# Kernel optimization log

Hardware: AMD Instinct MI355X
Metric: run time of the kernel (lower is better)

Reference implementation:

```python
import jax, jax.numpy as jnp
import numpy as np

B, S, H = 2, 2048, 2048
NH, HD = 16, 128


def _rope_tables(seq_len, dim, base=10000.0):
    inv_freq = 1.0 / (base ** (np.arange(0, dim, 2, dtype=np.float32) / dim))
    t = np.arange(seq_len, dtype=np.float32)
    freqs = np.outer(t, inv_freq)                      # [S, dim/2]
    emb = np.concatenate([freqs, freqs], axis=-1)      # [S, dim] (HF convention)
    return jnp.asarray(np.cos(emb)), jnp.asarray(np.sin(emb))


def setup_inputs() -> dict:
    key = jax.random.key(0)
    k1, k2, k3, k4, k5 = jax.random.split(key, 5)
    hidden_states = jax.random.normal(k1, (B, S, H), dtype=jnp.float32)
    # additive causal mask, broadcast over heads: (B, 1, S, S)
    causal = jnp.tril(jnp.ones((S, S), dtype=bool))
    attention_mask = jnp.where(causal, 0.0, -1e9).astype(jnp.float32)
    attention_mask = jnp.broadcast_to(attention_mask[None, None], (B, 1, S, S))
    rope_cos, rope_sin = _rope_tables(S, HD)
    scale = 1.0 / np.sqrt(H)
    Wq = jax.random.normal(k2, (H, H), dtype=jnp.float32) * scale
    Wk = jax.random.normal(k3, (H, H), dtype=jnp.float32) * scale
    Wv = jax.random.normal(k4, (H, H), dtype=jnp.float32) * scale
    Wo = jax.random.normal(k5, (H, H), dtype=jnp.float32) * scale
    return dict(hidden_states=hidden_states, attention_mask=attention_mask,
                rope_cos=rope_cos, rope_sin=rope_sin, Wq=Wq, Wk=Wk, Wv=Wv, Wo=Wo)


def _rotate_half(x):
    half = x.shape[-1] // 2
    return jnp.concatenate([-x[..., half:], x[..., :half]], axis=-1)


def reference(hidden_states, attention_mask, rope_cos, rope_sin, Wq, Wk, Wv, Wo):
    bsz, q_len, _ = hidden_states.shape
    scaling = HD ** -0.5
    # projections (torch Linear: y = x @ W.T)
    q = (hidden_states @ Wq.T).reshape(bsz, q_len, NH, HD).transpose(0, 2, 1, 3)
    k = (hidden_states @ Wk.T).reshape(bsz, q_len, NH, HD).transpose(0, 2, 1, 3)
    v = (hidden_states @ Wv.T).reshape(bsz, q_len, NH, HD).transpose(0, 2, 1, 3)
    # RoPE (rotate_half convention)
    cos = rope_cos[None, None]  # [1,1,S,HD]
    sin = rope_sin[None, None]
    q = q * cos + _rotate_half(q) * sin
    k = k * cos + _rotate_half(k) * sin
    # attention
    scores = jnp.einsum('bhqd,bhkd->bhqk', q, k) * scaling + attention_mask
    attn = jax.nn.softmax(scores.astype(jnp.float32), axis=-1).astype(q.dtype)
    out = jnp.einsum('bhqk,bhkd->bhqd', attn, v)
    out = out.transpose(0, 2, 1, 3).reshape(bsz, q_len, NH * HD)
    return out @ Wo.T
```

## Files before the change

kernel.cpp:

```cpp
#include <hip/hip_runtime.h>
#include <hip/hip_bf16.h>

typedef __bf16 bf16;
typedef __attribute__((ext_vector_type(8))) __bf16 bf16x8;
typedef __attribute__((ext_vector_type(4))) __bf16 bf16x4;
typedef __attribute__((ext_vector_type(4))) float f32x4;

#define BB 2
#define SS 2048
#define HH 2048
#define NH 16
#define HD 128

#define GLOAD_LDS16(g, l)                                                  \
    __builtin_amdgcn_global_load_lds(                                      \
        (const __attribute__((address_space(1))) void*)(g),                \
        (__attribute__((address_space(3))) void*)(l), 16, 0, 0)

__global__ __launch_bounds__(256) void cast_all(const float* __restrict__ hs,
                                                const float* __restrict__ Wq,
                                                const float* __restrict__ Wk,
                                                const float* __restrict__ Wv,
                                                const float* __restrict__ Wo,
                                                bf16* __restrict__ Xb,
                                                bf16* __restrict__ Wqkv,
                                                bf16* __restrict__ Wob) {
    const int XE4 = (BB * SS * HH) / 4;
    const int WE4 = (HH * HH) / 4;
    int i = blockIdx.x * 256 + threadIdx.x;
    const float* src;
    bf16* dst;
    int off;
    if (i < XE4) { src = hs; dst = Xb; off = i; }
    else if (i < XE4 + WE4) { src = Wq; dst = Wqkv; off = i - XE4; }
    else if (i < XE4 + 2 * WE4) { src = Wk; dst = Wqkv + (size_t)HH * HH; off = i - XE4 - WE4; }
    else if (i < XE4 + 3 * WE4) { src = Wv; dst = Wqkv + 2 * (size_t)HH * HH; off = i - XE4 - 2 * WE4; }
    else { src = Wo; dst = Wob; off = i - XE4 - 3 * WE4; }
    f32x4 v = *reinterpret_cast<const f32x4*>(src + (size_t)off * 4);
    bf16x4 o;
    o[0] = (bf16)v[0]; o[1] = (bf16)v[1]; o[2] = (bf16)v[2]; o[3] = (bf16)v[3];
    *reinterpret_cast<bf16x4*>(dst + (size_t)off * 4) = o;
}

__global__ __launch_bounds__(512, 2) void gemm256_qkv(const bf16* __restrict__ A,
                                                      const bf16* __restrict__ B,
                                                      bf16* __restrict__ Cb,
                                                      int M, int N, int K) {
    __shared__ bf16 LA[2][256 * 64];
    __shared__ bf16 LB[2][192 * 64];
    const int tid = threadIdx.x, lane = tid & 63, wave = tid >> 6;
    const int l15 = lane & 15, lhi = lane >> 4;
    const int wr = wave >> 2, wc = wave & 3;
    const int NBY = M >> 8;
    const int cpx = gridDim.x >> 3;
    const int wg = (blockIdx.x & 7) * cpx + (blockIdx.x >> 3);
    const int m0 = (wg & 15) * 256, n0 = (wg >> 4) * 192;
    const int NK = K >> 6;
    const int xorR = (l15 & 7) << 4;

    auto stageA = [&](int buf, int t, int h) {
        const int k0 = t << 6;
#pragma unroll
        for (int j = 0; j < 2; ++j) {
            int Xw = (h * 128 + j * 64 + wave * 8) << 7;
            int X = Xw + lane * 16;
            int T = X ^ (((X >> 7) & 7) << 4);
            GLOAD_LDS16(&A[(size_t)(m0 + (T >> 7)) * K + k0 + ((T & 127) >> 1)],
                        (char*)LA[buf] + Xw);
        }
    };
    auto stageB = [&](int buf, int t, int s) {
        const int k0 = t << 6;
        int row_base = (wave >> 1) * 48 + s * 16 + (wave & 1) * 8;
        int Xw = row_base << 7;
        int X = Xw + lane * 16;
        int T = X ^ (((X >> 7) & 7) << 4);
        GLOAD_LDS16(&B[(size_t)(n0 + (T >> 7)) * K + k0 + ((T & 127) >> 1)],
                    (char*)LB[buf] + Xw);
    };

    f32x4 acc[8][3] = {};

    stageA(0, 0, 0); stageA(0, 0, 1);
    stageB(0, 0, 0); stageB(0, 0, 1); stageB(0, 0, 2);
    stageA(1, 1, 0); stageA(1, 1, 1);
    stageB(1, 1, 0); stageB(1, 1, 1);
    asm volatile("s_waitcnt vmcnt(6)" ::: "memory");
    __builtin_amdgcn_s_barrier();

    bf16x8 af[8][2], bv[2];

#pragma unroll 1
    for (int t = 0; t < NK; ++t) {
        const int buf = t & 1;
        char* lA = (char*)LA[buf];
        char* lB = (char*)LB[buf];

#pragma unroll
        for (int mf = 0; mf < 8; ++mf)
#pragma unroll
            for (int ks = 0; ks < 2; ++ks) {
                int T = ((wr * 128 + mf * 16 + l15) << 7) + ks * 64 + lhi * 16;
                af[mf][ks] = *reinterpret_cast<const bf16x8*>(lA + (T ^ xorR));
            }
#pragma unroll
        for (int ks = 0; ks < 2; ++ks) {
            int T = ((wc * 48 + l15) << 7) + ks * 64 + lhi * 16;
            bv[ks] = *reinterpret_cast<const bf16x8*>(lB + (T ^ xorR));
        }
        if (t + 1 < NK) stageB(buf ^ 1, t + 1, 2);
        __builtin_amdgcn_s_barrier();
        __builtin_amdgcn_s_setprio(1);
#pragma unroll
        for (int mf = 0; mf < 8; ++mf)
#pragma unroll
            for (int ks = 0; ks < 2; ++ks)
                acc[mf][0] = __builtin_amdgcn_mfma_f32_16x16x32_bf16(af[mf][ks], bv[ks], acc[mf][0], 0, 0, 0);
        __builtin_amdgcn_s_setprio(0);
        __builtin_amdgcn_s_barrier();

#pragma unroll
        for (int ks = 0; ks < 2; ++ks) {
            int T = ((wc * 48 + 16 + l15) << 7) + ks * 64 + lhi * 16;
            bv[ks] = *reinterpret_cast<const bf16x8*>(lB + (T ^ xorR));
        }
        if (t + 2 < NK) { stageB(buf, t + 2, 0); stageA(buf, t + 2, 0); }
        __builtin_amdgcn_s_barrier();
        __builtin_amdgcn_s_setprio(1);
#pragma unroll
        for (int mf = 0; mf < 8; ++mf)
#pragma unroll
            for (int ks = 0; ks < 2; ++ks)
                acc[mf][1] = __builtin_amdgcn_mfma_f32_16x16x32_bf16(af[mf][ks], bv[ks], acc[mf][1], 0, 0, 0);
        __builtin_amdgcn_s_setprio(0);
        __builtin_amdgcn_s_barrier();

#pragma unroll
        for (int ks = 0; ks < 2; ++ks) {
            int T = ((wc * 48 + 32 + l15) << 7) + ks * 64 + lhi * 16;
            bv[ks] = *reinterpret_cast<const bf16x8*>(lB + (T ^ xorR));
        }
        if (t + 2 < NK) { stageB(buf, t + 2, 1); stageA(buf, t + 2, 1); }
        __builtin_amdgcn_s_barrier();
        __builtin_amdgcn_s_setprio(1);
#pragma unroll
        for (int mf = 0; mf < 8; ++mf)
#pragma unroll
            for (int ks = 0; ks < 2; ++ks)
                acc[mf][2] = __builtin_amdgcn_mfma_f32_16x16x32_bf16(af[mf][ks], bv[ks], acc[mf][2], 0, 0, 0);
        __builtin_amdgcn_s_setprio(0);
        if (t + 2 < NK) {
            asm volatile("s_waitcnt vmcnt(6)" ::: "memory");
        } else if (t + 2 == NK) {
            asm volatile("s_waitcnt vmcnt(0)" ::: "memory");
        }
        __builtin_amdgcn_s_barrier();
    }

#pragma unroll
    for (int mf = 0; mf < 8; ++mf)
#pragma unroll
        for (int nsl = 0; nsl < 3; ++nsl)
#pragma unroll
            for (int r = 0; r < 4; ++r) {
                int gm = m0 + wr * 128 + mf * 16 + lhi * 4 + r;
                int gn = n0 + wc * 48 + nsl * 16 + l15;
                int proj = gn >> 11, n2 = gn & 2047;
                int b = gm >> 11, s = gm & (SS - 1);
                int h = n2 >> 7, d = n2 & (HD - 1);
                Cb[((size_t)proj << 23) + ((((size_t)(b * NH + h)) * SS + s) << 7) + d] =
                    (bf16)acc[mf][nsl][r];
            }
}

__global__ __launch_bounds__(256) void gemm_bt(const bf16* __restrict__ A,
                                               const bf16* __restrict__ B,
                                               float* __restrict__ Cf,
                                               int M, int N, int K) {
    __shared__ bf16 As[128 * 64];
    __shared__ bf16 Bs[128 * 64];
    const int tid = threadIdx.x;
    const int lane = tid & 63, wave = tid >> 6;
    const int l15 = lane & 15, lhi = lane >> 4;
    const int m0 = blockIdx.y * 128, n0 = blockIdx.x * 128;
    const int wm = (wave >> 1) * 64, wn = (wave & 1) * 64;
    const int lrow = lane >> 3;
    const int lcol = (lane & 7) * 8;

    f32x4 acc[4][4] = {};

    for (int k0 = 0; k0 < K; k0 += 64) {
#pragma unroll
        for (int j = 0; j < 4; ++j) {
            const int c = wave * 4 + j;
            const int row = c * 8 + lrow;
            GLOAD_LDS16(&A[(size_t)(m0 + row) * K + k0 + lcol], &As[c * 512]);
            GLOAD_LDS16(&B[(size_t)(n0 + row) * K + k0 + lcol], &Bs[c * 512]);
        }
        __syncthreads();
#pragma unroll
        for (int ks = 0; ks < 2; ++ks) {
            bf16x8 af[4], bfr[4];
#pragma unroll
            for (int i = 0; i < 4; ++i)
                af[i] = *reinterpret_cast<const bf16x8*>(&As[(wm + i * 16 + l15) * 64 + ks * 32 + 8 * lhi]);
#pragma unroll
            for (int j = 0; j < 4; ++j)
                bfr[j] = *reinterpret_cast<const bf16x8*>(&Bs[(wn + j * 16 + l15) * 64 + ks * 32 + 8 * lhi]);
#pragma unroll
            for (int i = 0; i < 4; ++i)
#pragma unroll
                for (int j = 0; j < 4; ++j)
                    acc[i][j] = __builtin_amdgcn_mfma_f32_16x16x32_bf16(af[i], bfr[j], acc[i][j], 0, 0, 0);
        }
        __syncthreads();
    }

#pragma unroll
    for (int i = 0; i < 4; ++i)
#pragma unroll
        for (int j = 0; j < 4; ++j)
#pragma unroll
            for (int r = 0; r < 4; ++r) {
                int gm = m0 + wm + i * 16 + lhi * 4 + r;
                int gn = n0 + wn + j * 16 + l15;
                Cf[(size_t)gm * N + gn] = acc[i][j][r];
            }
}

__global__ __launch_bounds__(256) void rope_tv(bf16* __restrict__ Qh,
                                               bf16* __restrict__ Kh,
                                               const float* __restrict__ cosT,
                                               const float* __restrict__ sinT,
                                               const bf16* __restrict__ Vh,
                                               bf16* __restrict__ Vt) {
    __shared__ bf16 T[64 * 64];
    const int tid = threadIdx.x;
    if (blockIdx.x < 2048) {
        int idx = blockIdx.x * 256 + tid;
        int g = idx & 7;
        int s = (idx >> 3) & (SS - 1);
        int head = idx >> 14;
        int d0 = g * 8;
        size_t base = ((size_t)head * SS + s) * HD;
        f32x4 ca = *reinterpret_cast<const f32x4*>(&cosT[s * HD + d0]);
        f32x4 cb = *reinterpret_cast<const f32x4*>(&cosT[s * HD + d0 + 4]);
        f32x4 sa = *reinterpret_cast<const f32x4*>(&sinT[s * HD + d0]);
        f32x4 sb = *reinterpret_cast<const f32x4*>(&sinT[s * HD + d0 + 4]);
        bf16x8 ql = *reinterpret_cast<const bf16x8*>(&Qh[base + d0]);
        bf16x8 qh = *reinterpret_cast<const bf16x8*>(&Qh[base + 64 + d0]);
        bf16x8 kl = *reinterpret_cast<const bf16x8*>(&Kh[base + d0]);
        bf16x8 kh = *reinterpret_cast<const bf16x8*>(&Kh[base + 64 + d0]);
        bf16x8 qlo, qhi, klo, khi;
#pragma unroll
        for (int j = 0; j < 8; ++j) {
            float c = (j < 4) ? ca[j] : cb[j - 4];
            float sn = (j < 4) ? sa[j] : sb[j - 4];
            float q0 = (float)ql[j], q1 = (float)qh[j];
            float k0 = (float)kl[j], k1 = (float)kh[j];
            qlo[j] = (bf16)(q0 * c - q1 * sn);
            qhi[j] = (bf16)(q1 * c + q0 * sn);
            klo[j] = (bf16)(k0 * c - k1 * sn);
            khi[j] = (bf16)(k1 * c + k0 * sn);
        }
        *reinterpret_cast<bf16x8*>(&Qh[base + d0]) = qlo;
        *reinterpret_cast<bf16x8*>(&Qh[base + 64 + d0]) = qhi;
        *reinterpret_cast<bf16x8*>(&Kh[base + d0]) = klo;
        *reinterpret_cast<bf16x8*>(&Kh[base + 64 + d0]) = khi;
    } else {
        const int b2 = blockIdx.x - 2048;
        const int s0 = (b2 & 31) * 64;
        const int d0 = ((b2 >> 5) & 1) * 64;
        const int head = b2 >> 6;
        const bf16* src = Vh + ((size_t)head * SS) * HD;
        bf16* dst = Vt + ((size_t)head * HD) * SS;

#pragma unroll
        for (int i = 0; i < 2; ++i) {
            int id = tid + i * 256;
            int r = id >> 3, c16 = id & 7;
            bf16x8 v = *reinterpret_cast<const bf16x8*>(&src[(size_t)(s0 + r) * HD + d0 + c16 * 8]);
            int sw = c16 ^ ((r ^ (r >> 3)) & 7);
            *reinterpret_cast<bf16x8*>((char*)T + r * 128 + sw * 16) = v;
        }
        __syncthreads();
#pragma unroll
        for (int i = 0; i < 2; ++i) {
            int id = tid + i * 256;
            int dr = id >> 3, sc8 = (id & 7) * 8;
            bf16x8 o;
#pragma unroll
            for (int j = 0; j < 8; ++j) {
                int r = sc8 + j;
                int sw = (dr >> 3) ^ ((r ^ (r >> 3)) & 7);
                o[j] = *reinterpret_cast<const bf16*>((char*)T + r * 128 + sw * 16 + (dr & 7) * 2);
            }
            *reinterpret_cast<bf16x8*>(&dst[(size_t)(d0 + dr) * SS + s0 + sc8]) = o;
        }
    }
}

__global__ __launch_bounds__(512) void attn_kernel(const bf16* __restrict__ Q,
                                                   const bf16* __restrict__ K,
                                                   const bf16* __restrict__ Vt,
                                                   bf16* __restrict__ Ob) {
    __shared__ bf16 Ks[2][64 * 128];
    __shared__ bf16 Vs[2][128 * 64];
    __shared__ bf16 Ps[8][16 * 72];

    const int tid = threadIdx.x, lane = tid & 63, wave = tid >> 6;
    const int l15 = lane & 15, lhi = lane >> 4;
    const int bid = blockIdx.x;
    const int orig = (bid & 7) * 32 + (bid >> 3);
    const int head = orig >> 3;
    const int pi = orig & 7;
    const int b = head >> 4, h = head & (NH - 1);
    const size_t hb = (size_t)head * SS * HD;
    const bf16* Vth = Vt + (size_t)head * HD * SS;
    const float cexp = 0.08838834764831845f * 1.4426950408889634f;
    const float THR = 62.0f;

    auto stageKV = [&](int buf, int kv0) {
#pragma unroll
        for (int j = 0; j < 2; ++j) {
            int Xw = (j * 8 + wave) << 10;
            int X = Xw + lane * 16;
            int T = X ^ (((X >> 8) & 7) << 4);
            GLOAD_LDS16(&K[hb + (size_t)(kv0 + (T >> 8)) * HD + ((T & 255) >> 1)],
                        (char*)Ks[buf] + Xw);
        }
#pragma unroll
        for (int j = 0; j < 2; ++j) {
            int Xw = (j * 8 + wave) << 10;
            int X = Xw + lane * 16;
            int T = X ^ (((X >> 7) & 7) << 4);
            GLOAD_LDS16(&Vth[(size_t)(T >> 7) * SS + kv0 + ((T & 127) >> 1)],
                        (char*)Vs[buf] + Xw);
        }
    };

#pragma unroll 1
    for (int part = 0; part < 2; ++part) {
        const int t = part ? (15 - pi) : pi;
        const int q0 = t * 128;
        const int qw = q0 + wave * 16;
        const int nkv = 2 * t + 2;

        bf16x8 qf[4];
#pragma unroll
        for (int ks = 0; ks < 4; ++ks)
            qf[ks] = *reinterpret_cast<const bf16x8*>(
                &Q[hb + (size_t)(qw + l15) * HD + ks * 32 + 8 * lhi]);

        f32x4 oacc[8] = {};
        float Mr[4], Lp[4];
#pragma unroll
        for (int r = 0; r < 4; ++r) { Mr[r] = -INFINITY; Lp[r] = 0.f; }

        stageKV(0, 0);
        asm volatile("s_waitcnt vmcnt(0)" ::: "memory");
        __builtin_amdgcn_s_barrier();

        for (int it = 0; it < nkv; ++it) {
            const int cur = it & 1;
            if (it + 1 < nkv) stageKV(cur ^ 1, (it + 1) * 64);

            f32x4 sf[4] = {};
#pragma unroll
            for (int ks = 0; ks < 4; ++ks) {
#pragma unroll
                for (int ne = 0; ne < 4; ++ne) {
                    int row = ne * 16 + l15;
                    bf16x8 kf = *reinterpret_cast<const bf16x8*>(
                        (const char*)Ks[cur] + ((row * 256 + (ks * 4 + lhi) * 16) ^ ((row & 7) << 4)));
                    sf[ne] = __builtin_amdgcn_mfma_f32_16x16x32_bf16(qf[ks], kf, sf[ne], 0, 0, 0);
                }
            }

            if (it >= nkv - 2) {
#pragma unroll
                for (int ne = 0; ne < 4; ++ne)
#pragma unroll
                    for (int r = 0; r < 4; ++r) {
                        int gq = qw + lhi * 4 + r;
                        int gk = it * 64 + ne * 16 + l15;
                        if (gk > gq) sf[ne][r] = -INFINITY;
                    }
            }

            float lm[4];
#pragma unroll
            for (int r = 0; r < 4; ++r)
                lm[r] = fmaxf(fmaxf(sf[0][r], sf[1][r]), fmaxf(sf[2][r], sf[3][r]));
            bool need = (lm[0] > Mr[0] + THR) || (lm[1] > Mr[1] + THR) ||
                        (lm[2] > Mr[2] + THR) || (lm[3] > Mr[3] + THR);
            if (__any(need)) {
                float rmax[4] = {lm[0], lm[1], lm[2], lm[3]};
#pragma unroll
                for (int m = 1; m < 16; m <<= 1)
#pragma unroll
                    for (int r = 0; r < 4; ++r)
                        rmax[r] = fmaxf(rmax[r], __shfl_xor(rmax[r], m));
#pragma unroll
                for (int r = 0; r < 4; ++r) {
                    float nM = fmaxf(Mr[r], rmax[r]);
                    float scf = __builtin_amdgcn_exp2f((Mr[r] - nM) * cexp);
                    Mr[r] = nM;
                    Lp[r] *= scf;
#pragma unroll
                    for (int nf = 0; nf < 8; ++nf) oacc[nf][r] *= scf;
                }
            }
#pragma unroll
            for (int ne = 0; ne < 4; ++ne)
#pragma unroll
                for (int r = 0; r < 4; ++r) {
                    float p = __builtin_amdgcn_exp2f((sf[ne][r] - Mr[r]) * cexp);
                    Lp[r] += p;
                    Ps[wave][(lhi * 4 + r) * 72 + ne * 16 + l15] = (bf16)p;
                }

#pragma unroll
            for (int ks = 0; ks < 2; ++ks) {
                bf16x8 pa = *reinterpret_cast<const bf16x8*>(
                    &Ps[wave][l15 * 72 + ks * 32 + 8 * lhi]);
#pragma unroll
                for (int nf = 0; nf < 8; ++nf) {
                    int row = nf * 16 + l15;
                    bf16x8 vb = *reinterpret_cast<const bf16x8*>(
                        (const char*)Vs[cur] + ((row * 128 + (ks * 4 + lhi) * 16) ^ ((row & 7) << 4)));
                    oacc[nf] = __builtin_amdgcn_mfma_f32_16x16x32_bf16(pa, vb, oacc[nf], 0, 0, 0);
                }
            }

            asm volatile("s_waitcnt vmcnt(0)" ::: "memory");
            __builtin_amdgcn_s_barrier();
        }

#pragma unroll
        for (int m = 1; m < 16; m <<= 1)
#pragma unroll
            for (int r = 0; r < 4; ++r)
                Lp[r] += __shfl_xor(Lp[r], m);
        float inv[4];
#pragma unroll
        for (int r = 0; r < 4; ++r) inv[r] = 1.f / Lp[r];
#pragma unroll
        for (int nf = 0; nf < 8; ++nf)
#pragma unroll
            for (int r = 0; r < 4; ++r) {
                int s = qw + lhi * 4 + r;
                int d = nf * 16 + l15;
                Ob[((size_t)(b * SS + s)) * HH + h * HD + d] = (bf16)(oacc[nf][r] * inv[r]);
            }
    }
}

extern "C" void kernel_launch(void* const* d_in, const int* in_sizes, int n_in,
                              void* d_out, int out_size, void* d_ws, size_t ws_size,
                              hipStream_t stream) {
    const float* hs   = (const float*)d_in[0];
    const float* cosT = (const float*)d_in[2];
    const float* sinT = (const float*)d_in[3];
    const float* Wq   = (const float*)d_in[4];
    const float* Wk   = (const float*)d_in[5];
    const float* Wv   = (const float*)d_in[6];
    const float* Wo   = (const float*)d_in[7];
    float* out = (float*)d_out;

    char* w = (char*)d_ws;
    auto alloc = [&](size_t bytes) {
        char* p = w;
        w += (bytes + 255) & ~(size_t)255;
        return p;
    };
    const size_t XE = (size_t)BB * SS * HH;
    const size_t WE = (size_t)HH * HH;
    bf16* Xb   = (bf16*)alloc(XE * 2);
    bf16* Wqkv = (bf16*)alloc(3 * WE * 2);
    bf16* Wob  = (bf16*)alloc(WE * 2);
    bf16* QKV  = (bf16*)alloc(3 * XE * 2);
    bf16* Vtg  = (bf16*)alloc(XE * 2);
    bf16* Ob   = (bf16*)alloc(XE * 2);

    const int M = BB * SS;
    bf16* Qh = QKV;
    bf16* Kh = QKV + XE;
    bf16* Vh = QKV + 2 * XE;

    {
        int total4 = (int)((XE + 4 * WE) / 4);
        cast_all<<<(total4 + 255) / 256, 256, 0, stream>>>(hs, Wq, Wk, Wv, Wo, Xb, Wqkv, Wob);
    }

    gemm256_qkv<<<512, 512, 0, stream>>>(Xb, Wqkv, QKV, M, 3 * HH, HH);

    rope_tv<<<4096, 256, 0, stream>>>(Qh, Kh, cosT, sinT, Vh, Vtg);

    attn_kernel<<<256, 512, 0, stream>>>(Qh, Kh, Vtg, Ob);

    dim3 ogrid(HH / 128, M / 128);
    gemm_bt<<<ogrid, 256, 0, stream>>>(Ob, Wob, out, M, HH, HH);
}
```

Measured before the change: 261.3 us.

## Use pipelined 256x128 output GEMM and 32-row-per-wave attention tiles

Replaces the simple 128x128 output-projection GEMM with a double-buffered 256x128 tile kernel using swizzled LDS, prefetching two k-steps ahead, and priority hints around MFMA bursts, mirroring the QKV GEMM design. Attention now runs 4 waves per block, each handling 32 query rows (two MFMA row fragments), so each K/V LDS fragment load feeds twice as many MFMAs. The aim is more data reuse per LDS and global load and better overlap of memory with compute. The cost is more registers per wave and fewer waves per attention block, which may lower occupancy and latency hiding.

```diff
diff --git a/kernel.cpp b/kernel.cpp
--- a/kernel.cpp
+++ b/kernel.cpp
@@ -51,7 +51,6 @@
     const int tid = threadIdx.x, lane = tid & 63, wave = tid >> 6;
     const int l15 = lane & 15, lhi = lane >> 4;
     const int wr = wave >> 2, wc = wave & 3;
-    const int NBY = M >> 8;
     const int cpx = gridDim.x >> 3;
     const int wg = (blockIdx.x & 7) * cpx + (blockIdx.x >> 3);
     const int m0 = (wg & 15) * 256, n0 = (wg >> 4) * 192;
@@ -173,58 +172,111 @@
             }
 }
 
-__global__ __launch_bounds__(256) void gemm_bt(const bf16* __restrict__ A,
-                                               const bf16* __restrict__ B,
-                                               float* __restrict__ Cf,
-                                               int M, int N, int K) {
-    __shared__ bf16 As[128 * 64];
-    __shared__ bf16 Bs[128 * 64];
-    const int tid = threadIdx.x;
-    const int lane = tid & 63, wave = tid >> 6;
+__global__ __launch_bounds__(512, 2) void gemm_op(const bf16* __restrict__ A,
+                                                  const bf16* __restrict__ B,
+                                                  float* __restrict__ Cf,
+                                                  int M, int N, int K) {
+    __shared__ bf16 LA[2][256 * 64];
+    __shared__ bf16 LB[2][128 * 64];
+    const int tid = threadIdx.x, lane = tid & 63, wave = tid >> 6;
     const int l15 = lane & 15, lhi = lane >> 4;
-    const int m0 = blockIdx.y * 128, n0 = blockIdx.x * 128;
-    const int wm = (wave >> 1) * 64, wn = (wave & 1) * 64;
-    const int lrow = lane >> 3;
-    const int lcol = (lane & 7) * 8;
-
-    f32x4 acc[4][4] = {};
-
-    for (int k0 = 0; k0 < K; k0 += 64) {
-#pragma unroll
-        for (int j = 0; j < 4; ++j) {
-            const int c = wave * 4 + j;
-            const int row = c * 8 + lrow;
-            GLOAD_LDS16(&A[(size_t)(m0 + row) * K + k0 + lcol], &As[c * 512]);
-            GLOAD_LDS16(&B[(size_t)(n0 + row) * K + k0 + lcol], &Bs[c * 512]);
-        }
-        __syncthreads();
+    const int wr = wave >> 2, wc = wave & 3;
+    const int cpx = gridDim.x >> 3;
+    const int wg = (blockIdx.x & 7) * cpx + (blockIdx.x >> 3);
+    const int m0 = (wg & 15) * 256, n0 = (wg >> 4) * 128;
+    const int NK = K >> 6;
+    const int xorR = (l15 & 7) << 4;
+
+    auto stageA = [&](int buf, int t, int h) {
+        const int k0 = t << 6;
+#pragma unroll
+        for (int j = 0; j < 2; ++j) {
+            int Xw = (h * 128 + j * 64 + wave * 8) << 7;
+            int X = Xw + lane * 16;
+            int T = X ^ (((X >> 7) & 7) << 4);
+            GLOAD_LDS16(&A[(size_t)(m0 + (T >> 7)) * K + k0 + ((T & 127) >> 1)],
+                        (char*)LA[buf] + Xw);
+        }
+    };
+    auto stageB = [&](int buf, int t, int s) {
+        const int k0 = t << 6;
+        int row_base = (wave >> 1) * 32 + s * 16 + (wave & 1) * 8;
+        int Xw = row_base << 7;
+        int X = Xw + lane * 16;
+        int T = X ^ (((X >> 7) & 7) << 4);
+        GLOAD_LDS16(&B[(size_t)(n0 + (T >> 7)) * K + k0 + ((T & 127) >> 1)],
+                    (char*)LB[buf] + Xw);
+    };
+
+    f32x4 acc[8][2] = {};
+
+    stageA(0, 0, 0); stageA(0, 0, 1); stageB(0, 0, 0); stageB(0, 0, 1);
+    stageA(1, 1, 0); stageA(1, 1, 1); stageB(1, 1, 0);
+    asm volatile("s_waitcnt vmcnt(5)" ::: "memory");
+    __builtin_amdgcn_s_barrier();
+
+    bf16x8 af[8][2], bv[2];
+
+#pragma unroll 1
+    for (int t = 0; t < NK; ++t) {
+        const int buf = t & 1;
+        char* lA = (char*)LA[buf];
+        char* lB = (char*)LB[buf];
+
+#pragma unroll
+        for (int mf = 0; mf < 8; ++mf)
+#pragma unroll
+            for (int ks = 0; ks < 2; ++ks) {
+                int T = ((wr * 128 + mf * 16 + l15) << 7) + ks * 64 + lhi * 16;
+                af[mf][ks] = *reinterpret_cast<const bf16x8*>(lA + (T ^ xorR));
+            }
 #pragma unroll
         for (int ks = 0; ks < 2; ++ks) {
-            bf16x8 af[4], bfr[4];
-#pragma unroll
-            for (int i = 0; i < 4; ++i)
-                af[i] = *reinterpret_cast<const bf16x8*>(&As[(wm + i * 16 + l15) * 64 + ks * 32 + 8 * lhi]);
-#pragma unroll
-            for (int j = 0; j < 4; ++j)
-                bfr[j] = *reinterpret_cast<const bf16x8*>(&Bs[(wn + j * 16 + l15) * 64 + ks * 32 + 8 * lhi]);
-#pragma unroll
-            for (int i = 0; i < 4; ++i)
-#pragma unroll
-                for (int j = 0; j < 4; ++j)
-                    acc[i][j] = __builtin_amdgcn_mfma_f32_16x16x32_bf16(af[i], bfr[j], acc[i][j], 0, 0, 0);
-        }
-        __syncthreads();
+            int T = ((wc * 32 + l15) << 7) + ks * 64 + lhi * 16;
+            bv[ks] = *reinterpret_cast<const bf16x8*>(lB + (T ^ xorR));
+        }
+        if (t + 1 < NK) stageB(buf ^ 1, t + 1, 1);
+        __builtin_amdgcn_s_barrier();
+        __builtin_amdgcn_s_setprio(1);
+#pragma unroll
+        for (int mf = 0; mf < 8; ++mf)
+#pragma unroll
+            for (int ks = 0; ks < 2; ++ks)
+                acc[mf][0] = __builtin_amdgcn_mfma_f32_16x16x32_bf16(af[mf][ks], bv[ks], acc[mf][0], 0, 0, 0);
+        __builtin_amdgcn_s_setprio(0);
+        __builtin_amdgcn_s_barrier();
+
+#pragma unroll
+        for (int ks = 0; ks < 2; ++ks) {
+            int T = ((wc * 32 + 16 + l15) << 7) + ks * 64 + lhi * 16;
+            bv[ks] = *reinterpret_cast<const bf16x8*>(lB + (T ^ xorR));
+        }
+        if (t + 2 < NK) { stageB(buf, t + 2, 0); stageA(buf, t + 2, 0); stageA(buf, t + 2, 1); }
+        __builtin_amdgcn_s_barrier();
+        __builtin_amdgcn_s_setprio(1);
+#pragma unroll
+        for (int mf = 0; mf < 8; ++mf)
+#pragma unroll
+            for (int ks = 0; ks < 2; ++ks)
+                acc[mf][1] = __builtin_amdgcn_mfma_f32_16x16x32_bf16(af[mf][ks], bv[ks], acc[mf][1], 0, 0, 0);
+        __builtin_amdgcn_s_setprio(0);
+        if (t + 2 < NK) {
+            asm volatile("s_waitcnt vmcnt(5)" ::: "memory");
+        } else {
+            asm volatile("s_waitcnt vmcnt(0)" ::: "memory");
+        }
+        __builtin_amdgcn_s_barrier();
     }
 
 #pragma unroll
-    for (int i = 0; i < 4; ++i)
-#pragma unroll
-        for (int j = 0; j < 4; ++j)
+    for (int mf = 0; mf < 8; ++mf)
+#pragma unroll
+        for (int nsl = 0; nsl < 2; ++nsl)
 #pragma unroll
             for (int r = 0; r < 4; ++r) {
-                int gm = m0 + wm + i * 16 + lhi * 4 + r;
-                int gn = n0 + wn + j * 16 + l15;
-                Cf[(size_t)gm * N + gn] = acc[i][j][r];
+                int gm = m0 + wr * 128 + mf * 16 + lhi * 4 + r;
+                int gn = n0 + wc * 32 + nsl * 16 + l15;
+                Cf[(size_t)gm * N + gn] = acc[mf][nsl][r];
             }
 }
 
@@ -300,13 +352,13 @@
     }
 }
 
-__global__ __launch_bounds__(512) void attn_kernel(const bf16* __restrict__ Q,
+__global__ __launch_bounds__(256) void attn_kernel(const bf16* __restrict__ Q,
                                                    const bf16* __restrict__ K,
                                                    const bf16* __restrict__ Vt,
                                                    bf16* __restrict__ Ob) {
     __shared__ bf16 Ks[2][64 * 128];
     __shared__ bf16 Vs[2][128 * 64];
-    __shared__ bf16 Ps[8][16 * 72];
+    __shared__ bf16 Ps[4][32 * 72];
 
     const int tid = threadIdx.x, lane = tid & 63, wave = tid >> 6;
     const int l15 = lane & 15, lhi = lane >> 4;
@@ -322,16 +374,16 @@
 
     auto stageKV = [&](int buf, int kv0) {
 #pragma unroll
-        for (int j = 0; j < 2; ++j) {
-            int Xw = (j * 8 + wave) << 10;
+        for (int j = 0; j < 4; ++j) {
+            int Xw = (j * 4 + wave) << 10;
             int X = Xw + lane * 16;
             int T = X ^ (((X >> 8) & 7) << 4);
             GLOAD_LDS16(&K[hb + (size_t)(kv0 + (T >> 8)) * HD + ((T & 255) >> 1)],
                         (char*)Ks[buf] + Xw);
         }
 #pragma unroll
-        for (int j = 0; j < 2; ++j) {
-            int Xw = (j * 8 + wave) << 10;
+        for (int j = 0; j < 4; ++j) {
+            int Xw = (j * 4 + wave) << 10;
             int X = Xw + lane * 16;
             int T = X ^ (((X >> 7) & 7) << 4);
             GLOAD_LDS16(&Vth[(size_t)(T >> 7) * SS + kv0 + ((T & 127) >> 1)],
@@ -343,19 +395,23 @@
     for (int part = 0; part < 2; ++part) {
         const int t = part ? (15 - pi) : pi;
         const int q0 = t * 128;
-        const int qw = q0 + wave * 16;
+        const int qw0 = q0 + wave * 32;
         const int nkv = 2 * t + 2;
 
-        bf16x8 qf[4];
-#pragma unroll
-        for (int ks = 0; ks < 4; ++ks)
-            qf[ks] = *reinterpret_cast<const bf16x8*>(
-                &Q[hb + (size_t)(qw + l15) * HD + ks * 32 + 8 * lhi]);
-
-        f32x4 oacc[8] = {};
-        float Mr[4], Lp[4];
-#pragma unroll
-        for (int r = 0; r < 4; ++r) { Mr[r] = -INFINITY; Lp[r] = 0.f; }
+        bf16x8 qf[2][4];
+#pragma unroll
+        for (int mf = 0; mf < 2; ++mf)
+#pragma unroll
+            for (int ks = 0; ks < 4; ++ks)
+                qf[mf][ks] = *reinterpret_cast<const bf16x8*>(
+                    &Q[hb + (size_t)(qw0 + mf * 16 + l15) * HD + ks * 32 + 8 * lhi]);
+
+        f32x4 oacc[2][8] = {};
+        float Mr[2][4], Lp[2][4];
+#pragma unroll
+        for (int mf = 0; mf < 2; ++mf)
+#pragma unroll
+            for (int r = 0; r < 4; ++r) { Mr[mf][r] = -INFINITY; Lp[mf][r] = 0.f; }
 
         stageKV(0, 0);
         asm volatile("s_waitcnt vmcnt(0)" ::: "memory");
@@ -365,7 +421,7 @@
             const int cur = it & 1;
             if (it + 1 < nkv) stageKV(cur ^ 1, (it + 1) * 64);
 
-            f32x4 sf[4] = {};
+            f32x4 sf[2][4] = {};
 #pragma unroll
             for (int ks = 0; ks < 4; ++ks) {
 #pragma unroll
@@ -373,63 +429,84 @@
                     int row = ne * 16 + l15;
                     bf16x8 kf = *reinterpret_cast<const bf16x8*>(
                         (const char*)Ks[cur] + ((row * 256 + (ks * 4 + lhi) * 16) ^ ((row & 7) << 4)));
-                    sf[ne] = __builtin_amdgcn_mfma_f32_16x16x32_bf16(qf[ks], kf, sf[ne], 0, 0, 0);
+#pragma unroll
+                    for (int mf = 0; mf < 2; ++mf)
+                        sf[mf][ne] = __builtin_amdgcn_mfma_f32_16x16x32_bf16(qf[mf][ks], kf, sf[mf][ne], 0, 0, 0);
                 }
             }
 
             if (it >= nkv - 2) {
 #pragma unroll
+                for (int mf = 0; mf < 2; ++mf)
+#pragma unroll
+                    for (int ne = 0; ne < 4; ++ne)
+#pragma unroll
+                        for (int r = 0; r < 4; ++r) {
+                            int gq = qw0 + mf * 16 + lhi * 4 + r;
+                            int gk = it * 64 + ne * 16 + l15;
+                            if (gk > gq) sf[mf][ne][r] = -INFINITY;
+                        }
+            }
+
+            float lm[2][4];
+            bool need = false;
+#pragma unroll
+            for (int mf = 0; mf < 2; ++mf)
+#pragma unroll
+                for (int r = 0; r < 4; ++r) {
+                    lm[mf][r] = fmaxf(fmaxf(sf[mf][0][r], sf[mf][1][r]),
+                                      fmaxf(sf[mf][2][r], sf[mf][3][r]));
+                    need = need || (lm[mf][r] > Mr[mf][r] + THR);
+                }
+            if (__any(need)) {
+                float rmax[2][4];
+#pragma unroll
+                for (int mf = 0; mf < 2; ++mf)
+#pragma unroll
+                    for (int r = 0; r < 4; ++r) rmax[mf][r] = lm[mf][r];
+#pragma unroll
+                for (int m = 1; m < 16; m <<= 1)
+#pragma unroll
+                    for (int mf = 0; mf < 2; ++mf)
+#pragma unroll
+                        for (int r = 0; r < 4; ++r)
+                            rmax[mf][r] = fmaxf(rmax[mf][r], __shfl_xor(rmax[mf][r], m));
+#pragma unroll
+                for (int mf = 0; mf < 2; ++mf)
+#pragma unroll
+                    for (int r = 0; r < 4; ++r) {
+                        float nM = fmaxf(Mr[mf][r], rmax[mf][r]);
+                        float scf = __builtin_amdgcn_exp2f((Mr[mf][r] - nM) * cexp);
+                        Mr[mf][r] = nM;
+                        Lp[mf][r] *= scf;
+#pragma unroll
+                        for (int nf = 0; nf < 8; ++nf) oacc[mf][nf][r] *= scf;
+                    }
+            }
+#pragma unroll
+            for (int mf = 0; mf < 2; ++mf)
+#pragma unroll
                 for (int ne = 0; ne < 4; ++ne)
 #pragma unroll
                     for (int r = 0; r < 4; ++r) {
-                        int gq = qw + lhi * 4 + r;
-                        int gk = it * 64 + ne * 16 + l15;
-                        if (gk > gq) sf[ne][r] = -INFINITY;
+                        float p = __builtin_amdgcn_exp2f((sf[mf][ne][r] - Mr[mf][r]) * cexp);
+                        Lp[mf][r] += p;
+                        Ps[wave][(mf * 16 + lhi * 4 + r) * 72 + ne * 16 + l15] = (bf16)p;
                     }
-            }
-
-            float lm[4];
-#pragma unroll
-            for (int r = 0; r < 4; ++r)
-                lm[r] = fmaxf(fmaxf(sf[0][r], sf[1][r]), fmaxf(sf[2][r], sf[3][r]));
-            bool need = (lm[0] > Mr[0] + THR) || (lm[1] > Mr[1] + THR) ||
-                        (lm[2] > Mr[2] + THR) || (lm[3] > Mr[3] + THR);
-            if (__any(need)) {
-                float rmax[4] = {lm[0], lm[1], lm[2], lm[3]};
-#pragma unroll
-                for (int m = 1; m < 16; m <<= 1)
-#pragma unroll
-                    for (int r = 0; r < 4; ++r)
-                        rmax[r] = fmaxf(rmax[r], __shfl_xor(rmax[r], m));
-#pragma unroll
-                for (int r = 0; r < 4; ++r) {
-                    float nM = fmaxf(Mr[r], rmax[r]);
-                    float scf = __builtin_amdgcn_exp2f((Mr[r] - nM) * cexp);
-                    Mr[r] = nM;
-                    Lp[r] *= scf;
-#pragma unroll
-                    for (int nf = 0; nf < 8; ++nf) oacc[nf][r] *= scf;
-                }
-            }
-#pragma unroll
-            for (int ne = 0; ne < 4; ++ne)
-#pragma unroll
-                for (int r = 0; r < 4; ++r) {
-                    float p = __builtin_amdgcn_exp2f((sf[ne][r] - Mr[r]) * cexp);
-                    Lp[r] += p;
-                    Ps[wave][(lhi * 4 + r) * 72 + ne * 16 + l15] = (bf16)p;
-                }
 
 #pragma unroll
             for (int ks = 0; ks < 2; ++ks) {
-                bf16x8 pa = *reinterpret_cast<const bf16x8*>(
-                    &Ps[wave][l15 * 72 + ks * 32 + 8 * lhi]);
+                bf16x8 pa0 = *reinterpret_cast<const bf16x8*>(
+                    &Ps[wave][(l15) * 72 + ks * 32 + 8 * lhi]);
+                bf16x8 pa1 = *reinterpret_cast<const bf16x8*>(
+                    &Ps[wave][(16 + l15) * 72 + ks * 32 + 8 * lhi]);
 #pragma unroll
                 for (int nf = 0; nf < 8; ++nf) {
                     int row = nf * 16 + l15;
                     bf16x8 vb = *reinterpret_cast<const bf16x8*>(
                         (const char*)Vs[cur] + ((row * 128 + (ks * 4 + lhi) * 16) ^ ((row & 7) << 4)));
-                    oacc[nf] = __builtin_amdgcn_mfma_f32_16x16x32_bf16(pa, vb, oacc[nf], 0, 0, 0);
+                    oacc[0][nf] = __builtin_amdgcn_mfma_f32_16x16x32_bf16(pa0, vb, oacc[0][nf], 0, 0, 0);
+                    oacc[1][nf] = __builtin_amdgcn_mfma_f32_16x16x32_bf16(pa1, vb, oacc[1][nf], 0, 0, 0);
                 }
             }
 
@@ -440,19 +517,24 @@
 #pragma unroll
         for (int m = 1; m < 16; m <<= 1)
 #pragma unroll
-            for (int r = 0; r < 4; ++r)
-                Lp[r] += __shfl_xor(Lp[r], m);
-        float inv[4];
-#pragma unroll
-        for (int r = 0; r < 4; ++r) inv[r] = 1.f / Lp[r];
-#pragma unroll
-        for (int nf = 0; nf < 8; ++nf)
-#pragma unroll
-            for (int r = 0; r < 4; ++r) {
-                int s = qw + lhi * 4 + r;
-                int d = nf * 16 + l15;
-                Ob[((size_t)(b * SS + s)) * HH + h * HD + d] = (bf16)(oacc[nf][r] * inv[r]);
-            }
+            for (int mf = 0; mf < 2; ++mf)
+#pragma unroll
+                for (int r = 0; r < 4; ++r)
+                    Lp[mf][r] += __shfl_xor(Lp[mf][r], m);
+#pragma unroll
+        for (int mf = 0; mf < 2; ++mf) {
+            float inv[4];
+#pragma unroll
+            for (int r = 0; r < 4; ++r) inv[r] = 1.f / Lp[mf][r];
+#pragma unroll
+            for (int nf = 0; nf < 8; ++nf)
+#pragma unroll
+                for (int r = 0; r < 4; ++r) {
+                    int s = qw0 + mf * 16 + lhi * 4 + r;
+                    int d = nf * 16 + l15;
+                    Ob[((size_t)(b * SS + s)) * HH + h * HD + d] = (bf16)(oacc[mf][nf][r] * inv[r]);
+                }
+        }
     }
 }
 
@@ -497,8 +579,7 @@
 
     rope_tv<<<4096, 256, 0, stream>>>(Qh, Kh, cosT, sinT, Vh, Vtg);
 
-    attn_kernel<<<256, 512, 0, stream>>>(Qh, Kh, Vtg, Ob);
-
-    dim3 ogrid(HH / 128, M / 128);
-    gemm_bt<<<ogrid, 256, 0, stream>>>(Ob, Wob, out, M, HH, HH);
+    attn_kernel<<<256, 256, 0, stream>>>(Qh, Kh, Vtg, Ob);
+
+    gemm_op<<<256, 512, 0, stream>>>(Ob, Wob, out, M, HH, HH);
 }
```

New measurement: 274.0 us. +4.8%, slower.
